# Performance work log

Measured on AMD Instinct MI355X. Metric: run time of the kernel, lower is better.

The kernel has to match this reference:

```python
import jax, jax.numpy as jnp
import numpy as np

N_NODES = 10000
N_EDGES = 320000
D_IN = 256
D_OUT = 256
NEG_SLOPE = 0.2


def setup_inputs() -> dict:
    key = jax.random.key(0)
    ks = jax.random.split(key, 8)
    feature = jax.random.normal(ks[0], (N_NODES, D_IN), dtype=jnp.float32)
    src = jax.random.randint(ks[1], (N_EDGES,), 0, N_NODES, dtype=jnp.int32)
    dst = jax.random.randint(ks[2], (N_EDGES,), 0, N_NODES, dtype=jnp.int32)
    # Xavier-ish scaled weights
    s = 1.0 / np.sqrt(D_IN)
    W_s = jax.random.normal(ks[3], (D_OUT, D_IN), dtype=jnp.float32) * s
    W_t = jax.random.normal(ks[4], (D_OUT, D_IN), dtype=jnp.float32) * s
    W_attn = jax.random.normal(ks[5], (1, D_OUT), dtype=jnp.float32) * (1.0 / np.sqrt(D_OUT))
    W_fc = jax.random.normal(ks[6], (D_OUT, D_IN), dtype=jnp.float32) * s
    b_fc = jnp.zeros((D_OUT,), dtype=jnp.float32)
    return {"feature": feature, "src": src, "dst": dst,
            "W_s": W_s, "W_t": W_t, "W_attn": W_attn,
            "W_fc": W_fc, "b_fc": b_fc}


def reference(feature, src, dst, W_s, W_t, W_attn, W_fc, b_fc):
    n = feature.shape[0]
    # Project at node level, then gather (same math as projecting gathered feats).
    proj_s = feature @ W_s.T          # [N, D_OUT]
    proj_t = feature @ W_t.T          # [N, D_OUT]
    # Edge attention logits: attn(LeakyReLU(h_dst + h_src))
    z = proj_s[src] + proj_t[dst]     # [E, D_OUT]
    z = jnp.where(z >= 0, z, NEG_SLOPE * z)
    e = (z @ W_attn.T)[:, 0]          # [E]
    # edge_softmax with norm_by='src': softmax over outgoing edges of each src node
    m = jax.ops.segment_max(e, src, num_segments=n)          # [N]
    m = jnp.where(jnp.isfinite(m), m, 0.0)                   # guard empty segments
    e_exp = jnp.exp(e - m[src])                               # [E]
    denom = jax.ops.segment_sum(e_exp, src, num_segments=n)  # [N]
    alpha = e_exp / denom[src]                                # [E]
    # message = src feature * alpha; reduce = sum at dst
    msg = feature[src] * alpha[:, None]                       # [E, D_IN]
    agg = jax.ops.segment_sum(msg, dst, num_segments=n)       # [N, D_IN]
    # final linear
    return agg @ W_fc.T + b_fc
```

## Files before the change

### kernel.cpp

```cpp
#include <hip/hip_runtime.h>
#include <math.h>

#define N_NODES 10000
#define N_EDGES 320000
#define D 256
#define NEG_SLOPE 0.2f
#define BCAP 96
#define BLOCK 256
#define NF4 (N_NODES * D / 4)
#define NW4 (256 * 256 / 4)
#define NTILE_M 157
#define NTILES (NTILE_M * 12)
#define FILL_BLOCKS ((N_EDGES + BLOCK - 1) / BLOCK)
#define APAD 264

typedef unsigned short ushortT;
typedef __attribute__((ext_vector_type(8))) short bf16x8;
typedef __attribute__((ext_vector_type(4))) float f32x4;

__device__ __forceinline__ unsigned short f2bf(float f) {
  unsigned int u = __float_as_uint(f);
  u += 0x7FFFu + ((u >> 16) & 1u);
  return (unsigned short)(u >> 16);
}
__device__ __forceinline__ float bf2f(unsigned short u) {
  return __uint_as_float((unsigned int)u << 16);
}

__global__ void prep_kernel(const float* __restrict__ feat,
                            const float* __restrict__ Ws,
                            const float* __restrict__ Wt,
                            const float* __restrict__ Wfc,
                            ushortT* __restrict__ featb,
                            ushortT* __restrict__ Wcat,
                            int* __restrict__ cnt,
                            float* __restrict__ denom) {
  const int g = blockIdx.x * blockDim.x + threadIdx.x;
  if (g < NF4) {
    float4 v = ((const float4*)feat)[g];
    ushort4 u;
    u.x = f2bf(v.x); u.y = f2bf(v.y); u.z = f2bf(v.z); u.w = f2bf(v.w);
    ((ushort4*)featb)[g] = u;
    return;
  }
  const int gi = g - NF4;
  if (gi < 3 * NW4) {
    const float* W = (gi < NW4) ? Ws : ((gi < 2 * NW4) ? Wt : Wfc);
    const int off = gi - ((gi < NW4) ? 0 : ((gi < 2 * NW4) ? NW4 : 2 * NW4));
    float4 v = ((const float4*)W)[off];
    ushort4 u;
    u.x = f2bf(v.x); u.y = f2bf(v.y); u.z = f2bf(v.z); u.w = f2bf(v.w);
    ((ushort4*)Wcat)[gi] = u;
    return;
  }
  const int gn = gi - 3 * NW4;
  if (gn < N_NODES) {
    cnt[gn] = 0;
    denom[gn] = 0.f;
  }
}

__global__ void fill_kernel(const int* __restrict__ src,
                            const int* __restrict__ dst,
                            int* __restrict__ cnt,
                            int* __restrict__ src_b) {
  const int i = blockIdx.x * blockDim.x + threadIdx.x;
  if (i >= N_EDGES) return;
  const int dn = dst[i];
  const int slot = atomicAdd(&cnt[dn], 1);
  if (slot < BCAP) src_b[dn * BCAP + slot] = src[i];
}

__global__ __launch_bounds__(256, 2) void proj_kernel(
    const ushortT* __restrict__ featb,
    const ushortT* __restrict__ Wcat,
    ushortT* __restrict__ ps, ushortT* __restrict__ pt,
    ushortT* __restrict__ fcp) {
  __shared__ ushortT Als[64][APAD];
  __shared__ ushortT Bls[64][APAD];

  const int p = blockIdx.x;
  const int m0 = (p / 12) * 64;
  const int by = p % 12;
  ushortT* outp = (by < 4) ? ps : ((by < 8) ? pt : fcp);
  const int col0 = (by & 3) * 64;
  const int n0 = by * 64;

  const int tid = threadIdx.x;
  const int wave = tid >> 6;
  const int lane = tid & 63;
  const int quad = lane >> 4;
  const int l16 = lane & 15;

  const int m_base_t = (wave & 1) * 32;
  const int wn = wave >> 1;

  const int tr = tid >> 2;
  const int tk = (tid & 3) * 64;
  const int gr = m0 + tr;
  const int wr = n0 + tr;
  const bf16x8 zero8 = {0, 0, 0, 0, 0, 0, 0, 0};
  bf16x8 av[8], bv[8];
#pragma unroll
  for (int i = 0; i < 8; ++i)
    av[i] = (gr < N_NODES) ? *(const bf16x8*)(featb + (size_t)gr * D + tk + 8 * i) : zero8;
#pragma unroll
  for (int i = 0; i < 8; ++i)
    bv[i] = *(const bf16x8*)(Wcat + (size_t)wr * D + tk + 8 * i);
#pragma unroll
  for (int i = 0; i < 8; ++i) *(bf16x8*)&Als[tr][tk + 8 * i] = av[i];
#pragma unroll
  for (int i = 0; i < 8; ++i) *(bf16x8*)&Bls[tr][tk + 8 * i] = bv[i];
  __syncthreads();

  f32x4 acc[2][2];
#pragma unroll
  for (int i = 0; i < 2; ++i)
#pragma unroll
    for (int j = 0; j < 2; ++j) acc[i][j] = (f32x4){0.f, 0.f, 0.f, 0.f};

  const int ar0 = m_base_t + l16;
  const int br0 = wn * 32 + l16;
#pragma unroll
  for (int kk = 0; kk < 8; ++kk) {
    const int ko = kk * 32 + quad * 8;
    bf16x8 a0 = *(const bf16x8*)&Als[ar0][ko];
    bf16x8 a1 = *(const bf16x8*)&Als[ar0 + 16][ko];
    bf16x8 b0 = *(const bf16x8*)&Bls[br0][ko];
    bf16x8 b1 = *(const bf16x8*)&Bls[br0 + 16][ko];
    acc[0][0] = __builtin_amdgcn_mfma_f32_16x16x32_bf16(a0, b0, acc[0][0], 0, 0, 0);
    acc[0][1] = __builtin_amdgcn_mfma_f32_16x16x32_bf16(a0, b1, acc[0][1], 0, 0, 0);
    acc[1][0] = __builtin_amdgcn_mfma_f32_16x16x32_bf16(a1, b0, acc[1][0], 0, 0, 0);
    acc[1][1] = __builtin_amdgcn_mfma_f32_16x16x32_bf16(a1, b1, acc[1][1], 0, 0, 0);
  }

#pragma unroll
  for (int mi = 0; mi < 2; ++mi) {
#pragma unroll
    for (int r = 0; r < 4; ++r) {
      const int row = m0 + m_base_t + mi * 16 + quad * 4 + r;
      if (row < N_NODES) {
#pragma unroll
        for (int ni = 0; ni < 2; ++ni) {
          const int col = col0 + wn * 32 + ni * 16 + l16;
          outp[(size_t)row * D + col] = f2bf(acc[mi][ni][r]);
        }
      }
    }
  }
}

__global__ __launch_bounds__(256) void logit_bucket_kernel(
    const ushortT* __restrict__ ps,
    const ushortT* __restrict__ pt,
    const int* __restrict__ cnt,
    const int* __restrict__ src_b,
    const float* __restrict__ Wattn,
    float* __restrict__ expv_b,
    float* __restrict__ denom) {
  const int n = blockIdx.x;
  const int cn = min(cnt[n], BCAP);
  if (cn == 0) return;
  const int wave = threadIdx.x >> 6;
  const int lane = threadIdx.x & 63;
  const int half = lane >> 5;
  const int l32 = lane & 31;
  const int grp = wave * 2 + half;
  const int base = n * BCAP;

  bf16x8 bu = *(const bf16x8*)(pt + (size_t)n * D + l32 * 8);
  float b[8], w[8];
  const float4 w0 = *(const float4*)(Wattn + l32 * 8);
  const float4 w1 = *(const float4*)(Wattn + l32 * 8 + 4);
  w[0] = w0.x; w[1] = w0.y; w[2] = w0.z; w[3] = w0.w;
  w[4] = w1.x; w[5] = w1.y; w[6] = w1.z; w[7] = w1.w;
#pragma unroll
  for (int i = 0; i < 8; ++i) b[i] = bf2f((unsigned short)bu[i]);

  int j = grp;
  for (; j + 24 < cn; j += 32) {
    const int s0 = src_b[base + j];
    const int s1 = src_b[base + j + 8];
    const int s2 = src_b[base + j + 16];
    const int s3 = src_b[base + j + 24];
    bf16x8 au0 = *(const bf16x8*)(ps + (size_t)s0 * D + l32 * 8);
    bf16x8 au1 = *(const bf16x8*)(ps + (size_t)s1 * D + l32 * 8);
    bf16x8 au2 = *(const bf16x8*)(ps + (size_t)s2 * D + l32 * 8);
    bf16x8 au3 = *(const bf16x8*)(ps + (size_t)s3 * D + l32 * 8);
    float sum0 = 0.f, sum1 = 0.f, sum2 = 0.f, sum3 = 0.f;
#pragma unroll
    for (int i = 0; i < 8; ++i) {
      float z0 = bf2f((unsigned short)au0[i]) + b[i];
      float z1 = bf2f((unsigned short)au1[i]) + b[i];
      float z2 = bf2f((unsigned short)au2[i]) + b[i];
      float z3 = bf2f((unsigned short)au3[i]) + b[i];
      z0 = fmaxf(z0, NEG_SLOPE * z0);
      z1 = fmaxf(z1, NEG_SLOPE * z1);
      z2 = fmaxf(z2, NEG_SLOPE * z2);
      z3 = fmaxf(z3, NEG_SLOPE * z3);
      sum0 = fmaf(w[i], z0, sum0);
      sum1 = fmaf(w[i], z1, sum1);
      sum2 = fmaf(w[i], z2, sum2);
      sum3 = fmaf(w[i], z3, sum3);
    }
#pragma unroll
    for (int off = 16; off > 0; off >>= 1) {
      sum0 += __shfl_down(sum0, off, 32);
      sum1 += __shfl_down(sum1, off, 32);
      sum2 += __shfl_down(sum2, off, 32);
      sum3 += __shfl_down(sum3, off, 32);
    }
    if (l32 == 0) {
      float ex0 = __expf(sum0), ex1 = __expf(sum1);
      float ex2 = __expf(sum2), ex3 = __expf(sum3);
      expv_b[base + j] = ex0;
      expv_b[base + j + 8] = ex1;
      expv_b[base + j + 16] = ex2;
      expv_b[base + j + 24] = ex3;
      atomicAdd(&denom[s0], ex0);
      atomicAdd(&denom[s1], ex1);
      atomicAdd(&denom[s2], ex2);
      atomicAdd(&denom[s3], ex3);
    }
  }
  for (; j < cn; j += 8) {
    const int s = src_b[base + j];
    bf16x8 au = *(const bf16x8*)(ps + (size_t)s * D + l32 * 8);
    float sum = 0.f;
#pragma unroll
    for (int i = 0; i < 8; ++i) {
      float z = bf2f((unsigned short)au[i]) + b[i];
      z = fmaxf(z, NEG_SLOPE * z);
      sum = fmaf(w[i], z, sum);
    }
#pragma unroll
    for (int off = 16; off > 0; off >>= 1) sum += __shfl_down(sum, off, 32);
    if (l32 == 0) {
      float ex = __expf(sum);
      expv_b[base + j] = ex;
      atomicAdd(&denom[s], ex);
    }
  }
}

__global__ __launch_bounds__(64) void prescale_kernel(
    const ushortT* __restrict__ fcp,
    const float* __restrict__ denom,
    ushortT* __restrict__ fcpsb) {
  const int n = blockIdx.x;
  const int t = threadIdx.x;
  const float inv = 1.0f / denom[n];
  ushort4 v = ((const ushort4*)(fcp + (size_t)n * D))[t];
  ushort4 o;
  o.x = f2bf(bf2f(v.x) * inv);
  o.y = f2bf(bf2f(v.y) * inv);
  o.z = f2bf(bf2f(v.z) * inv);
  o.w = f2bf(bf2f(v.w) * inv);
  ((ushort4*)(fcpsb + (size_t)n * D))[t] = o;
}

__global__ __launch_bounds__(256) void gather_agg_kernel(
    const ushortT* __restrict__ fcpsb,
    const int* __restrict__ cnt,
    const int* __restrict__ src_b,
    const float* __restrict__ expv_b,
    const float* __restrict__ b_fc,
    float* __restrict__ out) {
  __shared__ float red[8][D];
  const int n = blockIdx.x;
  const int tid = threadIdx.x;
  const int wave = tid >> 6;
  const int lane = tid & 63;
  const int half = lane >> 5;
  const int l32 = lane & 31;
  const int grp = wave * 2 + half;
  const int cn = min(cnt[n], BCAP);
  const int base = n * BCAP;

  float acc[8];
#pragma unroll
  for (int i = 0; i < 8; ++i) acc[i] = 0.f;

  int j = grp;
  for (; j + 24 < cn; j += 32) {
    const int s0 = src_b[base + j];
    const int s1 = src_b[base + j + 8];
    const int s2 = src_b[base + j + 16];
    const int s3 = src_b[base + j + 24];
    const float a0 = expv_b[base + j];
    const float a1 = expv_b[base + j + 8];
    const float a2 = expv_b[base + j + 16];
    const float a3 = expv_b[base + j + 24];
    bf16x8 f0 = *(const bf16x8*)(fcpsb + (size_t)s0 * D + l32 * 8);
    bf16x8 f1 = *(const bf16x8*)(fcpsb + (size_t)s1 * D + l32 * 8);
    bf16x8 f2 = *(const bf16x8*)(fcpsb + (size_t)s2 * D + l32 * 8);
    bf16x8 f3 = *(const bf16x8*)(fcpsb + (size_t)s3 * D + l32 * 8);
#pragma unroll
    for (int i = 0; i < 8; ++i) {
      acc[i] = fmaf(a0, bf2f((unsigned short)f0[i]), acc[i]);
      acc[i] = fmaf(a1, bf2f((unsigned short)f1[i]), acc[i]);
      acc[i] = fmaf(a2, bf2f((unsigned short)f2[i]), acc[i]);
      acc[i] = fmaf(a3, bf2f((unsigned short)f3[i]), acc[i]);
    }
  }
  for (; j < cn; j += 8) {
    const int s = src_b[base + j];
    const float a = expv_b[base + j];
    bf16x8 fu = *(const bf16x8*)(fcpsb + (size_t)s * D + l32 * 8);
#pragma unroll
    for (int i = 0; i < 8; ++i)
      acc[i] = fmaf(a, bf2f((unsigned short)fu[i]), acc[i]);
  }
  *(float4*)&red[grp][l32 * 8] = make_float4(acc[0], acc[1], acc[2], acc[3]);
  *(float4*)&red[grp][l32 * 8 + 4] = make_float4(acc[4], acc[5], acc[6], acc[7]);
  __syncthreads();
  float o = b_fc[tid];
#pragma unroll
  for (int g = 0; g < 8; ++g) o += red[g][tid];
  out[(size_t)n * D + tid] = o;
}

extern "C" void kernel_launch(void* const* d_in, const int* in_sizes, int n_in,
                              void* d_out, int out_size, void* d_ws, size_t ws_size,
                              hipStream_t stream) {
  const float* feat  = (const float*)d_in[0];
  const int*   src   = (const int*)d_in[1];
  const int*   dst   = (const int*)d_in[2];
  const float* Ws    = (const float*)d_in[3];
  const float* Wt    = (const float*)d_in[4];
  const float* Wattn = (const float*)d_in[5];
  const float* Wfc   = (const float*)d_in[6];
  const float* bfc   = (const float*)d_in[7];
  float* out = (float*)d_out;

  ushortT* ps    = (ushortT*)d_ws;
  ushortT* pt    = ps + (size_t)N_NODES * D;
  ushortT* fcp   = pt + (size_t)N_NODES * D;
  ushortT* featb = fcp + (size_t)N_NODES * D;
  ushortT* Wcat  = featb + (size_t)N_NODES * D;
  float* expv_b  = (float*)(Wcat + (size_t)768 * 256);
  float* denom   = expv_b + (size_t)N_NODES * BCAP;
  int*   cnt     = (int*)(denom + N_NODES);
  int*   src_b   = cnt + N_NODES;
  ushortT* fcpsb = featb;

  const int prep_items = NF4 + 3 * NW4 + N_NODES;
  prep_kernel<<<(prep_items + BLOCK - 1) / BLOCK, BLOCK, 0, stream>>>(
      feat, Ws, Wt, Wfc, featb, Wcat, cnt, denom);
  fill_kernel<<<FILL_BLOCKS, BLOCK, 0, stream>>>(src, dst, cnt, src_b);
  proj_kernel<<<NTILES, BLOCK, 0, stream>>>(featb, Wcat, ps, pt, fcp);
  logit_bucket_kernel<<<N_NODES, BLOCK, 0, stream>>>(ps, pt, cnt, src_b, Wattn, expv_b, denom);
  prescale_kernel<<<N_NODES, 64, 0, stream>>>(fcp, denom, fcpsb);
  gather_agg_kernel<<<N_NODES, BLOCK, 0, stream>>>(fcpsb, cnt, src_b, expv_b, bfc, out);
}
```

Measured before the change: 181.9 us.

## Fuse edge bucketing into projection GEMM, stage output via LDS, batch prescale

The edge-bucketing fill work now runs as extra blocks of the projection GEMM launch, removing one kernel launch and letting the atomic fill overlap with GEMM tiles. The GEMM epilogue writes results into an LDS tile first and then stores 16-byte vectors to global memory instead of scattered 2-byte stores. The prescale kernel now handles four nodes per 256-thread block instead of one node per 64-thread block. The extra LDS tile raises shared memory per block slightly, and the fill blocks now run with the GEMM kernel's launch bounds.

```diff
diff --git a/kernel.cpp b/kernel.cpp
--- a/kernel.cpp
+++ b/kernel.cpp
@@ -13,6 +13,7 @@
 #define NTILES (NTILE_M * 12)
 #define FILL_BLOCKS ((N_EDGES + BLOCK - 1) / BLOCK)
 #define APAD 264
+#define CPAD 66
 
 typedef unsigned short ushortT;
 typedef __attribute__((ext_vector_type(8))) short bf16x8;
@@ -60,26 +61,27 @@
   }
 }
 
-__global__ void fill_kernel(const int* __restrict__ src,
-                            const int* __restrict__ dst,
-                            int* __restrict__ cnt,
-                            int* __restrict__ src_b) {
-  const int i = blockIdx.x * blockDim.x + threadIdx.x;
-  if (i >= N_EDGES) return;
-  const int dn = dst[i];
-  const int slot = atomicAdd(&cnt[dn], 1);
-  if (slot < BCAP) src_b[dn * BCAP + slot] = src[i];
-}
-
-__global__ __launch_bounds__(256, 2) void proj_kernel(
+__global__ __launch_bounds__(256, 2) void proj_fill_kernel(
     const ushortT* __restrict__ featb,
     const ushortT* __restrict__ Wcat,
+    const int* __restrict__ src, const int* __restrict__ dst,
+    int* __restrict__ cnt, int* __restrict__ src_b,
     ushortT* __restrict__ ps, ushortT* __restrict__ pt,
     ushortT* __restrict__ fcp) {
   __shared__ ushortT Als[64][APAD];
   __shared__ ushortT Bls[64][APAD];
-
-  const int p = blockIdx.x;
+  __shared__ ushortT Cls[64][CPAD];
+
+  if (blockIdx.x < FILL_BLOCKS) {
+    const int i = blockIdx.x * BLOCK + threadIdx.x;
+    if (i < N_EDGES) {
+      const int dn = dst[i];
+      const int slot = atomicAdd(&cnt[dn], 1);
+      if (slot < BCAP) src_b[dn * BCAP + slot] = src[i];
+    }
+    return;
+  }
+  const int p = blockIdx.x - FILL_BLOCKS;
   const int m0 = (p / 12) * 64;
   const int by = p % 12;
   ushortT* outp = (by < 4) ? ps : ((by < 8) ? pt : fcp);
@@ -135,18 +137,23 @@
   }
 
 #pragma unroll
-  for (int mi = 0; mi < 2; ++mi) {
+  for (int mi = 0; mi < 2; ++mi)
 #pragma unroll
     for (int r = 0; r < 4; ++r) {
-      const int row = m0 + m_base_t + mi * 16 + quad * 4 + r;
-      if (row < N_NODES) {
-#pragma unroll
-        for (int ni = 0; ni < 2; ++ni) {
-          const int col = col0 + wn * 32 + ni * 16 + l16;
-          outp[(size_t)row * D + col] = f2bf(acc[mi][ni][r]);
-        }
-      }
-    }
+      const int row = m_base_t + mi * 16 + quad * 4 + r;
+#pragma unroll
+      for (int ni = 0; ni < 2; ++ni)
+        Cls[row][wn * 32 + ni * 16 + l16] = f2bf(acc[mi][ni][r]);
+    }
+  __syncthreads();
+#pragma unroll
+  for (int it = 0; it < 2; ++it) {
+    const int idx = tid + it * 256;
+    const int row = idx >> 3;
+    const int cc = (idx & 7) * 8;
+    const int grow = m0 + row;
+    if (grow < N_NODES)
+      *(bf16x8*)(outp + (size_t)grow * D + col0 + cc) = *(const bf16x8*)&Cls[row][cc];
   }
 }
 
@@ -243,12 +250,13 @@
   }
 }
 
-__global__ __launch_bounds__(64) void prescale_kernel(
+__global__ __launch_bounds__(256) void prescale_kernel(
     const ushortT* __restrict__ fcp,
     const float* __restrict__ denom,
     ushortT* __restrict__ fcpsb) {
-  const int n = blockIdx.x;
-  const int t = threadIdx.x;
+  const int n = blockIdx.x * 4 + (threadIdx.x >> 6);
+  if (n >= N_NODES) return;
+  const int t = threadIdx.x & 63;
   const float inv = 1.0f / denom[n];
   ushort4 v = ((const ushort4*)(fcp + (size_t)n * D))[t];
   ushort4 o;
@@ -347,9 +355,9 @@
   const int prep_items = NF4 + 3 * NW4 + N_NODES;
   prep_kernel<<<(prep_items + BLOCK - 1) / BLOCK, BLOCK, 0, stream>>>(
       feat, Ws, Wt, Wfc, featb, Wcat, cnt, denom);
-  fill_kernel<<<FILL_BLOCKS, BLOCK, 0, stream>>>(src, dst, cnt, src_b);
-  proj_kernel<<<NTILES, BLOCK, 0, stream>>>(featb, Wcat, ps, pt, fcp);
+  proj_fill_kernel<<<FILL_BLOCKS + NTILES, BLOCK, 0, stream>>>(
+      featb, Wcat, src, dst, cnt, src_b, ps, pt, fcp);
   logit_bucket_kernel<<<N_NODES, BLOCK, 0, stream>>>(ps, pt, cnt, src_b, Wattn, expv_b, denom);
-  prescale_kernel<<<N_NODES, 64, 0, stream>>>(fcp, denom, fcpsb);
+  prescale_kernel<<<(N_NODES + 3) / 4, BLOCK, 0, stream>>>(fcp, denom, fcpsb);
   gather_agg_kernel<<<N_NODES, BLOCK, 0, stream>>>(fcpsb, cnt, src_b, expv_b, bfc, out);
 }
```

Result: faster. 171.9 us (-5.5%).
